# Optimization experiments

Measured on AMD Instinct MI355X. Metric: run time of the kernel, lower is better.

The kernel has to match this reference:

```python
import jax, jax.numpy as jnp
import numpy as np

B, N, E, C, ND, MID, OUT = 4, 16384, 131072, 128, 3, 128, 128


def setup_inputs() -> dict:
    key = jax.random.key(0)
    ks = jax.random.split(key, 11)
    f = jax.random.normal(ks[0], (B, C, N), dtype=jnp.float32)
    nodes = jax.random.normal(ks[1], (B, N, ND), dtype=jnp.float32)
    node_weights = jax.random.uniform(ks[2], (B, N, 1), dtype=jnp.float32)  # positive quadrature weights
    edges_index = jax.random.randint(ks[3], (B, E, 2), 0, N)
    edge_gradient_weights = jax.random.normal(ks[4], (B, E, ND), dtype=jnp.float32) * 0.1
    mlp_w1 = jax.random.normal(ks[5], (MID, ND * C), dtype=jnp.float32) * 0.02
    mlp_b1 = jnp.zeros((MID,), dtype=jnp.float32)
    mlp_w2 = jax.random.normal(ks[6], (OUT, MID), dtype=jnp.float32) * 0.02
    mlp_b2 = jnp.zeros((OUT,), dtype=jnp.float32)
    L = jax.random.normal(ks[7], (ND, ND), dtype=jnp.float32) * 0.1  # Cholesky factor (scaled for non-degenerate exp)
    chol_bias = jnp.zeros((ND,), dtype=jnp.float32)
    return dict(f=f, nodes=nodes, node_weights=node_weights, edges_index=edges_index,
                edge_gradient_weights=edge_gradient_weights, mlp_w1=mlp_w1, mlp_b1=mlp_b1,
                mlp_w2=mlp_w2, mlp_b2=mlp_b2, L=L, chol_bias=chol_bias)


def reference(f, nodes, node_weights, edges_index, edge_gradient_weights,
              mlp_w1, mlp_b1, mlp_w2, mlp_b2, L, chol_bias):
    b, c, n = f.shape
    nd = edge_gradient_weights.shape[-1]
    bidx = jnp.arange(b)[:, None]
    src_g = edges_index[..., 0]
    tgt_g = edges_index[..., 1]

    # ---- compute_gradient: gather f[src]-f[tgt], weight by edge_gradient_weights, scatter-add to target ----
    fT = f.transpose(0, 2, 1)  # (B,N,C)
    df = jnp.take_along_axis(fT, src_g[..., None], axis=1) - jnp.take_along_axis(fT, tgt_g[..., None], axis=1)  # (B,E,C)
    msg = (df[:, :, :, None] * edge_gradient_weights[:, :, None, :]).reshape(b, df.shape[1], c * nd)  # 'bed,bec->becd'
    grad = jnp.zeros((b, n, c * nd), f.dtype).at[bidx, tgt_g].add(msg)
    g = grad.transpose(0, 2, 1)  # (B, C*nd, N)

    # ---- pointwise MLP over channel dim (Conv1d k=1 -> GELU -> Conv1d k=1) ----
    h = jnp.einsum('mk,bkn->bmn', mlp_w1, g) + mlp_b1[None, :, None]
    h = jax.nn.gelu(h, approximate=False)
    h = jnp.einsum('om,bmn->bon', mlp_w2, h) + mlp_b2[None, :, None]
    fo = h.transpose(0, 2, 1)  # (B,N,OUT)
    o = fo.shape[-1]

    # ---- Gaussian edge kernel via Cholesky PSD form, with self-edges appended ----
    self_e = jnp.broadcast_to(jnp.arange(n)[None, :], (b, n))
    src = jnp.concatenate([src_g, self_e], axis=-1)
    tgt = jnp.concatenate([tgt_g, self_e], axis=-1)
    f_src = jnp.take_along_axis(fo, src[..., None], axis=1)  # (B,E+N,OUT)
    d = jnp.take_along_axis(nodes, src[..., None], axis=1) - jnp.take_along_axis(nodes, tgt[..., None], axis=1)  # (B,E+N,nd)
    Sigma = L @ L.T  # positive semi-definite inverse covariance
    dS = d @ Sigma.T + chol_bias  # F.linear
    w_src = jnp.take_along_axis(node_weights, src[..., None], axis=1)[..., 0]  # (B,E+N)
    kernel = w_src * jnp.exp(-jnp.einsum('bed,bed->be', d, dS))

    # ---- scatter-add normalization and aggregation ----
    inv = 1.0 / jnp.zeros((b, n), f.dtype).at[bidx, tgt].add(kernel)
    out = jnp.zeros((b, n, o), f.dtype).at[bidx, tgt].add(f_src * kernel[..., None]) * inv[..., None]
    return out.transpose(0, 2, 1)  # (B,OUT,N)
```

## Files before the change

### kernel.cpp

```cpp
#include <hip/hip_runtime.h>
#include <hip/hip_bf16.h>

static constexpr int B   = 4;
static constexpr int N   = 16384;
static constexpr int E   = 131072;
static constexpr int C   = 128;
static constexpr int ND  = 3;
static constexpr int MID = 128;
static constexpr int OUT = 128;
static constexpr int K1  = C * ND;
static constexpr int NT  = 32;
static constexpr int K1P = 392;

typedef __attribute__((ext_vector_type(8))) short bf16x8;
typedef __attribute__((ext_vector_type(4))) float f32x4;

__device__ __forceinline__ ushort f2bf(float x) {
    union { float f; unsigned u; } v; v.f = x;
    return (ushort)((v.u + 0x7fffu + ((v.u >> 16) & 1u)) >> 16);
}
__device__ __forceinline__ float bf2f(ushort u) {
    union { unsigned u; float f; } v; v.u = (unsigned)u << 16;
    return v.f;
}

__global__ void k_front(const float* __restrict__ f, ushort* __restrict__ fT,
                        const int2* __restrict__ ei2, int* __restrict__ deg,
                        const float* __restrict__ W1, const float* __restrict__ W2,
                        const float* __restrict__ L, ushort* __restrict__ W1p,
                        ushort* __restrict__ W2p, float* __restrict__ Sig) {
    __shared__ float tile[32][33];
    int bid = blockIdx.x, tid = threadIdx.x;
    if (bid < 8192) {
        int bx = bid & 511, by = (bid >> 9) & 3, b = bid >> 11;
        int n0 = bx * 32, c0 = by * 32;
        const float* fb = f + (size_t)b * C * N;
        ushort* fTb = fT + (size_t)b * N * C;
        int tx = tid & 31, ty = tid >> 5;
        #pragma unroll
        for (int i = 0; i < 32; i += 8)
            tile[ty + i][tx] = fb[(size_t)(c0 + ty + i) * N + n0 + tx];
        __syncthreads();
        #pragma unroll
        for (int i = 0; i < 32; i += 8)
            fTb[(size_t)(n0 + ty + i) * C + c0 + tx] = f2bf(tile[tx][ty + i]);
    } else if (bid < 10240) {
        int idx = (bid - 8192) * 256 + tid;
        int b = idx >> 17;
        int tgt = ei2[idx].y;
        atomicAdd(&deg[b * N + tgt], 1);
    } else {
        int gid = (bid - 10240) * 256 + tid;
        for (int i = gid; i < 8 * 12 * 64 * 8; i += 64 * 256) {
            int j = i & 7, l = (i >> 3) & 63, t = (i >> 9) % 12, nt = (i >> 9) / 12;
            int n = nt * 16 + (l & 15);
            int k = t * 32 + ((l >> 4) & 3) * 8 + j;
            W1p[i] = f2bf(W1[n * K1 + k]);
        }
        {
            int i = gid;
            int j = i & 7, l = (i >> 3) & 63, t = (i >> 9) % 4, nt = (i >> 9) / 4;
            int n = nt * 16 + (l & 15);
            int k = t * 32 + ((l >> 4) & 3) * 8 + j;
            W2p[i] = f2bf(W2[n * MID + k]);
        }
        if (gid < 9) {
            int i = gid / 3, j = gid % 3;
            Sig[gid] = L[i * 3 + 0] * L[j * 3 + 0] + L[i * 3 + 1] * L[j * 3 + 1] +
                       L[i * 3 + 2] * L[j * 3 + 2];
        }
    }
}

__global__ void k_scan1(const int4* __restrict__ degv, int* __restrict__ rowptr,
                        int* __restrict__ bsum) {
    __shared__ int s[256];
    int blk = blockIdx.x, t = threadIdx.x;
    int4 d = degv[blk * 256 + t];
    s[t] = d.x + d.y + d.z + d.w;
    __syncthreads();
    for (int off = 1; off < 256; off <<= 1) {
        int v = s[t];
        int u = (t >= off) ? s[t - off] : 0;
        __syncthreads();
        s[t] = v + u;
        __syncthreads();
    }
    int excl = (t == 0) ? 0 : s[t - 1];
    if (t == 255) bsum[blk] = s[255];
    int4 w;
    w.x = excl;
    w.y = excl + d.x;
    w.z = w.y + d.y;
    w.w = w.z + d.z;
    ((int4*)rowptr)[blk * 256 + t] = w;
}

__global__ void k_scan2(int* __restrict__ bsum, int* __restrict__ rowptr) {
    __shared__ int s[64];
    int t = threadIdx.x;
    s[t] = bsum[t];
    __syncthreads();
    for (int off = 1; off < 64; off <<= 1) {
        int v = s[t];
        int u = (t >= off) ? s[t - off] : 0;
        __syncthreads();
        s[t] = v + u;
        __syncthreads();
    }
    bsum[t] = (t == 0) ? 0 : s[t - 1];
    if (t == 63) rowptr[B * N] = s[63];
}

__global__ void k_scan3(int4* __restrict__ rowv, const int* __restrict__ bsum) {
    int i = blockIdx.x * 256 + threadIdx.x;
    int add = bsum[i >> 8];
    int4 v = rowv[i];
    v.x += add; v.y += add; v.z += add; v.w += add;
    rowv[i] = v;
}

__global__ void k_fill_perm(const int2* __restrict__ ei2,
                            const int* __restrict__ rowptr,
                            int* __restrict__ cursor, int* __restrict__ perm) {
    int idx = blockIdx.x * 256 + threadIdx.x;
    int b = idx >> 17;
    int tgt = ei2[idx].y;
    int bn = b * N + tgt;
    int pos = atomicAdd(&cursor[bn], 1);
    perm[rowptr[bn] + pos] = idx;
}

__global__ void k_fill_expand(const int* __restrict__ perm,
                              const int2* __restrict__ ei2,
                              const float* __restrict__ egw,
                              const float* __restrict__ nodes,
                              const float* __restrict__ nw,
                              const float* __restrict__ Sig,
                              const float* __restrict__ cb,
                              float4* __restrict__ egwp, float2* __restrict__ ka2) {
    int o = blockIdx.x * 256 + threadIdx.x;
    int idx = perm[o];
    int b = idx >> 17;
    int2 e = ei2[idx];
    int src = e.x, tgt = e.y;
    const float* w = egw + (size_t)idx * ND;
    egwp[o] = make_float4(w[0], w[1], w[2], __int_as_float(src));
    const float* ns = nodes + ((size_t)b * N + src) * ND;
    const float* nt = nodes + ((size_t)b * N + tgt) * ND;
    float d0 = ns[0] - nt[0], d1 = ns[1] - nt[1], d2 = ns[2] - nt[2];
    float q = d0 * (Sig[0] * d0 + Sig[1] * d1 + Sig[2] * d2) +
              d1 * (Sig[3] * d0 + Sig[4] * d1 + Sig[5] * d2) +
              d2 * (Sig[6] * d0 + Sig[7] * d1 + Sig[8] * d2) +
              d0 * cb[0] + d1 * cb[1] + d2 * cb[2];
    ka2[o] = make_float2(nw[(size_t)b * N + src] * expf(-q), __int_as_float(src));
}

#define EDGE_FMA(W, U)                                                         \
    {                                                                          \
        float dx = bf2f(U.x) - ft.x, dy = bf2f(U.y) - ft.y,                    \
              dz = bf2f(U.z) - ft.z, dw = bf2f(U.w) - ft.w;                    \
        a0.x = fmaf(dx, W.x, a0.x); a0.y = fmaf(dy, W.x, a0.y);                \
        a0.z = fmaf(dz, W.x, a0.z); a0.w = fmaf(dw, W.x, a0.w);                \
        a1.x = fmaf(dx, W.y, a1.x); a1.y = fmaf(dy, W.y, a1.y);                \
        a1.z = fmaf(dz, W.y, a1.z); a1.w = fmaf(dw, W.y, a1.w);                \
        a2.x = fmaf(dx, W.z, a2.x); a2.y = fmaf(dy, W.z, a2.y);                \
        a2.z = fmaf(dz, W.z, a2.z); a2.w = fmaf(dw, W.z, a2.w);                \
    }

#define EDGE_LOAD(K)                                                           \
    float4 w##K = egwp[base + i + K];                                          \
    ushort4 u##K = *(const ushort4*)(fTb + (size_t)__float_as_int(w##K.w) * C + cg4);

__global__ __launch_bounds__(512, 5) void k_grad_mlp(
    const ushort* __restrict__ fT, const int* __restrict__ rowptr,
    const float4* __restrict__ egwp, const ushort* __restrict__ W1p,
    const float* __restrict__ b1, const ushort* __restrict__ W2p,
    const float* __restrict__ b2, ushort* __restrict__ fo) {
    __shared__ ushort g_s[NT][K1P];
    int tid = threadIdx.x;
    int bid = blockIdx.x;
    int swz = (bid & 7) * ((B * N / NT) >> 3) + (bid >> 3);
    int n0 = swz * NT;

    {
        int cg = tid & 31, s = tid >> 5;
        int cg4 = cg * 4;
        for (int jj = 0; jj < NT; jj += 16) {
            int j = jj + s;
            int n = n0 + j;
            const ushort* fTb = fT + (size_t)(n >> 14) * N * C;
            float4 ft;
            {
                ushort4 u = *(const ushort4*)(fT + (size_t)n * C + cg4);
                ft = make_float4(bf2f(u.x), bf2f(u.y), bf2f(u.z), bf2f(u.w));
            }
            int base = rowptr[n], cnt = rowptr[n + 1] - base;
            float4 a0 = make_float4(0.f, 0.f, 0.f, 0.f), a1 = a0, a2 = a0;
            int i = 0;
            for (; i + 8 <= cnt; i += 8) {
                EDGE_LOAD(0); EDGE_LOAD(1); EDGE_LOAD(2); EDGE_LOAD(3);
                EDGE_LOAD(4); EDGE_LOAD(5); EDGE_LOAD(6); EDGE_LOAD(7);
                EDGE_FMA(w0, u0); EDGE_FMA(w1, u1);
                EDGE_FMA(w2, u2); EDGE_FMA(w3, u3);
                EDGE_FMA(w4, u4); EDGE_FMA(w5, u5);
                EDGE_FMA(w6, u6); EDGE_FMA(w7, u7);
            }
            for (; i + 4 <= cnt; i += 4) {
                EDGE_LOAD(0); EDGE_LOAD(1); EDGE_LOAD(2); EDGE_LOAD(3);
                EDGE_FMA(w0, u0); EDGE_FMA(w1, u1);
                EDGE_FMA(w2, u2); EDGE_FMA(w3, u3);
            }
            for (; i < cnt; ++i) {
                EDGE_LOAD(0);
                EDGE_FMA(w0, u0);
            }
            unsigned p0 = (unsigned)f2bf(a0.x) | ((unsigned)f2bf(a1.x) << 16);
            unsigned p1 = (unsigned)f2bf(a2.x) | ((unsigned)f2bf(a0.y) << 16);
            unsigned p2 = (unsigned)f2bf(a1.y) | ((unsigned)f2bf(a2.y) << 16);
            unsigned p3 = (unsigned)f2bf(a0.z) | ((unsigned)f2bf(a1.z) << 16);
            unsigned p4 = (unsigned)f2bf(a2.z) | ((unsigned)f2bf(a0.w) << 16);
            unsigned p5 = (unsigned)f2bf(a1.w) | ((unsigned)f2bf(a2.w) << 16);
            uint2* dst = (uint2*)&g_s[j][cg * 12];
            dst[0] = make_uint2(p0, p1);
            dst[1] = make_uint2(p2, p3);
            dst[2] = make_uint2(p4, p5);
        }
    }
    __syncthreads();

    int wv = tid >> 6, ln = tid & 63, lr = ln & 15, lh = ln >> 4;
    int mt = wv & 1, nh = wv >> 1;
    bf16x8 a[12];
    {
        const ushort* grow = &g_s[mt * 16 + lr][0];
        #pragma unroll
        for (int t = 0; t < 12; ++t)
            a[t] = *(const bf16x8*)(grow + t * 32 + lh * 8);
    }
    __syncthreads();

    ushort(*h_s)[136] = (ushort(*)[136]) & g_s[0][0];
    const bf16x8* W1f = (const bf16x8*)W1p;
    #pragma unroll
    for (int q = 0; q < 2; ++q) {
        int nt = nh * 2 + q;
        float bb = b1[nt * 16 + lr];
        f32x4 c = {bb, bb, bb, bb};
        #pragma unroll
        for (int t = 0; t < 12; ++t)
            c = __builtin_amdgcn_mfma_f32_16x16x32_bf16(
                a[t], W1f[(nt * 12 + t) * 64 + ln], c, 0, 0, 0);
        #pragma unroll
        for (int r = 0; r < 4; ++r) {
            float x = c[r];
            x = 0.5f * x * (1.0f + erff(x * 0.70710678118654752f));
            h_s[mt * 16 + lh * 4 + r][nt * 16 + lr] = f2bf(x);
        }
    }
    __syncthreads();

    bf16x8 a2[4];
    {
        const ushort* hrow = &h_s[mt * 16 + lr][0];
        #pragma unroll
        for (int t = 0; t < 4; ++t)
            a2[t] = *(const bf16x8*)(hrow + t * 32 + lh * 8);
    }
    const bf16x8* W2f = (const bf16x8*)W2p;
    #pragma unroll
    for (int q = 0; q < 2; ++q) {
        int nt = nh * 2 + q;
        float bb = b2[nt * 16 + lr];
        f32x4 c = {bb, bb, bb, bb};
        #pragma unroll
        for (int t = 0; t < 4; ++t)
            c = __builtin_amdgcn_mfma_f32_16x16x32_bf16(
                a2[t], W2f[(nt * 4 + t) * 64 + ln], c, 0, 0, 0);
        #pragma unroll
        for (int r = 0; r < 4; ++r)
            fo[(size_t)(n0 + mt * 16 + lh * 4 + r) * OUT + nt * 16 + lr] = f2bf(c[r]);
    }
}

#define AGG_FMA(K, U)                                                          \
    {                                                                          \
        o.x = fmaf(bf2f(U.x), K.x, o.x); o.y = fmaf(bf2f(U.y), K.x, o.y);      \
        o.z = fmaf(bf2f(U.z), K.x, o.z); o.w = fmaf(bf2f(U.w), K.x, o.w);      \
        den += K.x;                                                            \
    }

__global__ __launch_bounds__(512, 5) void k_agg_t(const ushort* __restrict__ fo,
                                                  const float* __restrict__ nw,
                                                  const int* __restrict__ rowptr,
                                                  const float2* __restrict__ ka2,
                                                  float* __restrict__ out) {
    __shared__ float t[OUT][65];
    int tid = threadIdx.x;
    int cg4 = (tid & 31) * 4;
    int s = tid >> 5;
    int bid = blockIdx.x;
    int swz = (bid & 7) * ((B * N / 64) >> 3) + (bid >> 3);
    int n0 = swz * 64;
    int b = n0 >> 14, ncol0 = n0 & (N - 1);
    const ushort* fob = fo + (size_t)b * N * OUT;
    #pragma unroll
    for (int g = 0; g < 4; ++g) {
        int nl = g * 16 + s;
        int n = n0 + nl;
        int base = rowptr[n], cnt = rowptr[n + 1] - base;
        float4 o = make_float4(0.f, 0.f, 0.f, 0.f);
        float den = 0.f;
        int i = 0;
        for (; i + 4 <= cnt; i += 4) {
            float2 k0 = ka2[base + i];
            float2 k1 = ka2[base + i + 1];
            float2 k2 = ka2[base + i + 2];
            float2 k3 = ka2[base + i + 3];
            ushort4 u0 = *(const ushort4*)(fob + (size_t)__float_as_int(k0.y) * OUT + cg4);
            ushort4 u1 = *(const ushort4*)(fob + (size_t)__float_as_int(k1.y) * OUT + cg4);
            ushort4 u2 = *(const ushort4*)(fob + (size_t)__float_as_int(k2.y) * OUT + cg4);
            ushort4 u3 = *(const ushort4*)(fob + (size_t)__float_as_int(k3.y) * OUT + cg4);
            AGG_FMA(k0, u0);
            AGG_FMA(k1, u1);
            AGG_FMA(k2, u2);
            AGG_FMA(k3, u3);
        }
        for (; i < cnt; ++i) {
            float2 k0 = ka2[base + i];
            ushort4 u0 = *(const ushort4*)(fob + (size_t)__float_as_int(k0.y) * OUT + cg4);
            AGG_FMA(k0, u0);
        }
        float wn = nw[n];
        ushort4 uf = *(const ushort4*)(fo + (size_t)n * OUT + cg4);
        float inv = 1.f / (den + wn);
        t[cg4 + 0][nl] = (o.x + bf2f(uf.x) * wn) * inv;
        t[cg4 + 1][nl] = (o.y + bf2f(uf.y) * wn) * inv;
        t[cg4 + 2][nl] = (o.z + bf2f(uf.z) * wn) * inv;
        t[cg4 + 3][nl] = (o.w + bf2f(uf.w) * wn) * inv;
    }
    __syncthreads();
    #pragma unroll
    for (int i = 0; i < 16; ++i) {
        int idx = tid + i * 512;
        int o = idx >> 6, nl = idx & 63;
        out[((size_t)b * OUT + o) * N + ncol0 + nl] = t[o][nl];
    }
}

extern "C" void kernel_launch(void* const* d_in, const int* in_sizes, int n_in,
                              void* d_out, int out_size, void* d_ws, size_t ws_size,
                              hipStream_t stream) {
    const float* f     = (const float*)d_in[0];
    const float* nodes = (const float*)d_in[1];
    const float* nw    = (const float*)d_in[2];
    const int*   ei    = (const int*)d_in[3];
    const float* egw   = (const float*)d_in[4];
    const float* W1    = (const float*)d_in[5];
    const float* b1    = (const float*)d_in[6];
    const float* W2    = (const float*)d_in[7];
    const float* b2    = (const float*)d_in[8];
    const float* L     = (const float*)d_in[9];
    const float* cb    = (const float*)d_in[10];
    float* out = (float*)d_out;

    char* ws = (char*)d_ws;
    auto alloc = [&](size_t bytes) {
        void* p = ws;
        ws += (bytes + 255) & ~(size_t)255;
        return p;
    };
    ushort* fT     = (ushort*)alloc((size_t)B * N * C * 2);
    ushort* fo     = (ushort*)alloc((size_t)B * N * OUT * 2);
    ushort* W1p    = (ushort*)alloc((size_t)MID * K1 * 2);
    ushort* W2p    = (ushort*)alloc((size_t)OUT * MID * 2);
    float*  Sig    = (float*)alloc(16 * 4);
    int*    deg    = (int*)alloc((size_t)B * N * 4);
    int*    cursor = (int*)alloc((size_t)B * N * 4);
    int*    rowptr = (int*)alloc(((size_t)B * N + 4) * 4);
    int*    bsum   = (int*)alloc(64 * 4);
    int*    perm   = (int*)alloc((size_t)B * E * 4);
    float4* egwp   = (float4*)alloc((size_t)B * E * 16);
    float2* ka2    = (float2*)alloc((size_t)B * E * 8);

    hipMemsetAsync(deg, 0, (size_t)B * N * 4 * 2, stream);

    k_front<<<10304, 256, 0, stream>>>(f, fT, (const int2*)ei, deg, W1, W2, L,
                                       W1p, W2p, Sig);
    k_scan1<<<64, 256, 0, stream>>>((const int4*)deg, rowptr, bsum);
    k_scan2<<<1, 64, 0, stream>>>(bsum, rowptr);
    k_scan3<<<64, 256, 0, stream>>>((int4*)rowptr, bsum);
    k_fill_perm<<<(B * E) / 256, 256, 0, stream>>>((const int2*)ei, rowptr, cursor,
                                                   perm);
    k_fill_expand<<<(B * E) / 256, 256, 0, stream>>>(perm, (const int2*)ei, egw,
                                                     nodes, nw, Sig, cb, egwp, ka2);
    k_grad_mlp<<<(B * N) / NT, 512, 0, stream>>>(fT, rowptr, egwp, W1p, b1, W2p,
                                                 b2, fo);
    k_agg_t<<<(B * N) / 64, 512, 0, stream>>>(fo, nw, rowptr, ka2, out);
}
```

Before: 171.0 us.

## Dynamically assign nodes to half-waves via shared atomic counter in grad and agg kernels

Both the gradient+MLP kernel and the aggregation kernel now hand out nodes to each 32-lane group through an LDS atomic counter instead of a fixed strided assignment. This is meant to balance the uneven per-node edge counts (random graph degrees) across groups within a block. The 8-wide edge unroll in the gradient loop is also dropped, leaving the 4-wide loop, which may reduce register pressure but exposes less memory-level parallelism. It adds an atomic, a shuffle and a loop-carried dependency per node.

```diff
diff --git a/kernel.cpp b/kernel.cpp
--- a/kernel.cpp
+++ b/kernel.cpp
@@ -178,16 +178,24 @@
     const float* __restrict__ b1, const ushort* __restrict__ W2p,
     const float* __restrict__ b2, ushort* __restrict__ fo) {
     __shared__ ushort g_s[NT][K1P];
+    __shared__ int ctr;
     int tid = threadIdx.x;
     int bid = blockIdx.x;
     int swz = (bid & 7) * ((B * N / NT) >> 3) + (bid >> 3);
     int n0 = swz * NT;
 
+    if (tid == 0) ctr = 0;
+    __syncthreads();
+
     {
-        int cg = tid & 31, s = tid >> 5;
+        int cg = tid & 31;
         int cg4 = cg * 4;
-        for (int jj = 0; jj < NT; jj += 16) {
-            int j = jj + s;
+        bool lane0 = (cg == 0);
+        for (;;) {
+            int j;
+            if (lane0) j = atomicAdd(&ctr, 1);
+            j = __shfl(j, 0, 32);
+            if (j >= NT) break;
             int n = n0 + j;
             const ushort* fTb = fT + (size_t)(n >> 14) * N * C;
             float4 ft;
@@ -198,14 +206,6 @@
             int base = rowptr[n], cnt = rowptr[n + 1] - base;
             float4 a0 = make_float4(0.f, 0.f, 0.f, 0.f), a1 = a0, a2 = a0;
             int i = 0;
-            for (; i + 8 <= cnt; i += 8) {
-                EDGE_LOAD(0); EDGE_LOAD(1); EDGE_LOAD(2); EDGE_LOAD(3);
-                EDGE_LOAD(4); EDGE_LOAD(5); EDGE_LOAD(6); EDGE_LOAD(7);
-                EDGE_FMA(w0, u0); EDGE_FMA(w1, u1);
-                EDGE_FMA(w2, u2); EDGE_FMA(w3, u3);
-                EDGE_FMA(w4, u4); EDGE_FMA(w5, u5);
-                EDGE_FMA(w6, u6); EDGE_FMA(w7, u7);
-            }
             for (; i + 4 <= cnt; i += 4) {
                 EDGE_LOAD(0); EDGE_LOAD(1); EDGE_LOAD(2); EDGE_LOAD(3);
                 EDGE_FMA(w0, u0); EDGE_FMA(w1, u1);
@@ -296,17 +296,25 @@
                                                   const float2* __restrict__ ka2,
                                                   float* __restrict__ out) {
     __shared__ float t[OUT][65];
+    __shared__ int ctr;
     int tid = threadIdx.x;
-    int cg4 = (tid & 31) * 4;
-    int s = tid >> 5;
+    int cg = tid & 31;
+    int cg4 = cg * 4;
+    bool lane0 = (cg == 0);
     int bid = blockIdx.x;
     int swz = (bid & 7) * ((B * N / 64) >> 3) + (bid >> 3);
     int n0 = swz * 64;
     int b = n0 >> 14, ncol0 = n0 & (N - 1);
     const ushort* fob = fo + (size_t)b * N * OUT;
-    #pragma unroll
-    for (int g = 0; g < 4; ++g) {
-        int nl = g * 16 + s;
+
+    if (tid == 0) ctr = 0;
+    __syncthreads();
+
+    for (;;) {
+        int nl;
+        if (lane0) nl = atomicAdd(&ctr, 1);
+        nl = __shfl(nl, 0, 32);
+        if (nl >= 64) break;
         int n = n0 + nl;
         int base = rowptr[n], cnt = rowptr[n + 1] - base;
         float4 o = make_float4(0.f, 0.f, 0.f, 0.f);
```

Result: faster. 164.6 us (-3.7%).
